# Kernel optimization log

Hardware: AMD Instinct MI355X
Metric: run time of the kernel (lower is better)

## Reference

```python
import jax, jax.numpy as jnp
import numpy as np

HEADS = 8
DIM_HEAD = 40


def setup_inputs() -> dict:
    key = jax.random.key(0)
    ks = jax.random.split(key, 10)
    b, n, j, qd, cd = 8, 4096, 77, 320, 768
    inner = HEADS * DIM_HEAD  # 320
    x = jax.random.normal(ks[0], (b, n, qd), jnp.float32)
    embs = jax.random.normal(ks[1], (b, j, cd), jnp.float32)
    Wq = jax.random.normal(ks[2], (qd, inner), jnp.float32) * 0.02
    Wk = jax.random.normal(ks[3], (cd, inner), jnp.float32) * 0.02
    Wv = jax.random.normal(ks[4], (cd, inner), jnp.float32) * 0.02
    Wo = jax.random.normal(ks[5], (inner, qd), jnp.float32) * 0.02
    bo = jnp.zeros((qd,), jnp.float32)
    # per-query-token, per-key-token additive attention mask (float weights)
    cross_attn_mask = (jax.random.uniform(ks[6], (b, n, j)) < 0.5).astype(jnp.float32)
    strength = jnp.ones((1,), jnp.float32) * 0.8
    # captiontypes >= 0 marks valid key tokens; include some -1 (invalid)
    captiontypes = jax.random.randint(ks[7], (b, j), -1, 3).at[:, 0].set(0)
    global_prompt_mask = (jax.random.uniform(ks[8], (b, j)) > 0.05).at[:, 0].set(True)
    return {"x": x, "embs": embs, "Wq": Wq, "Wk": Wk, "Wv": Wv, "Wo": Wo,
            "bo": bo, "cross_attn_mask": cross_attn_mask, "strength": strength,
            "captiontypes": captiontypes, "global_prompt_mask": global_prompt_mask}


def _split_heads(t):
    # [b, n, h*d] -> [(b h), n, d], head index fastest (matches einops '(b h)')
    b, n, _ = t.shape
    return t.reshape(b, n, HEADS, DIM_HEAD).transpose(0, 2, 1, 3).reshape(b * HEADS, n, DIM_HEAD)


def reference(x, embs, Wq, Wk, Wv, Wo, bo, cross_attn_mask, strength,
              captiontypes, global_prompt_mask):
    b, n, _ = x.shape
    scale = DIM_HEAD ** -0.5
    q = _split_heads(x @ Wq).astype(jnp.float32)   # [(b h), n, d]
    k = _split_heads(embs @ Wk).astype(jnp.float32)  # [(b h), j, d]
    v = _split_heads(embs @ Wv)                      # [(b h), j, d]
    sim = jnp.einsum('bid,bjd->bij', q, k)           # [(b h), n, j] fp32

    NEG = -jnp.finfo(sim.dtype).max
    key_mask = captiontypes >= 0                     # [b, j]
    key_mask_bh = jnp.repeat(key_mask, HEADS, axis=0)[:, None, :]  # [(b h), 1, j]

    # masked std of sim over valid key positions (unbiased, ddof=1), no grad
    w = jnp.broadcast_to(key_mask_bh, sim.shape).astype(sim.dtype)
    cnt = jnp.sum(w)
    mean = jnp.sum(sim * w) / cnt
    var = jnp.sum(w * (sim - mean) ** 2) / (cnt - 1.0)
    simstd = jnp.sqrt(var)

    wf = cross_attn_mask * simstd * strength[0]      # [b, n, j]
    wf = jnp.where(global_prompt_mask[:, None, :], wf, NEG)
    wf = jnp.repeat(wf, HEADS, axis=0)               # [(b h), n, j]
    wf = jax.lax.stop_gradient(wf)

    sim = jnp.where(key_mask_bh, sim, NEG) + wf
    attn = jax.nn.softmax(sim * scale, axis=-1)
    out = jnp.einsum('bij,bjd->bid', attn, v)        # [(b h), n, d]
    out = out.reshape(b, HEADS, n, DIM_HEAD).transpose(0, 2, 1, 3).reshape(b, n, HEADS * DIM_HEAD)
    return out @ Wo + bo
```

## Files before the change

### kernel.cpp

```cpp
#include <hip/hip_runtime.h>
#include <hip/hip_bf16.h>
#include <math.h>

#define HEADS 8
#define DIMH 40
#define BB 8
#define NN 4096
#define JJ 77
#define CDIM 768
#define INNER 320
#define NEGF (-3.4028234663852886e38f)

using bf16 = __hip_bfloat16;
using f32x4 = __attribute__((ext_vector_type(4))) float;
using bf16x8 = __attribute__((ext_vector_type(8))) short;
using ushort8 = __attribute__((ext_vector_type(8))) unsigned short;
using ushort4v = __attribute__((ext_vector_type(4))) unsigned short;

__device__ __forceinline__ unsigned short f2u(float f){
    bf16 t = __float2bfloat16(f);
    return *reinterpret_cast<unsigned short*>(&t);
}
__device__ __forceinline__ float u2f(unsigned short u){
    unsigned int w = ((unsigned int)u) << 16;
    return __uint_as_float(w);
}

struct Stats { int validcnt; int gflag; float simstd; };

__global__ void prep_kernel(const int* ct, const int* gpm, Stats* st){
    __shared__ int sflag, scnt;
    if(threadIdx.x==0){ sflag=0; scnt=0; }
    __syncthreads();
    int lflag=0, lcnt=0;
    for(int i=threadIdx.x;i<154;i+=blockDim.x){
        int g = gpm[i];
        if(g!=0 && g!=1) lflag=1;
    }
    for(int i=threadIdx.x;i<BB*JJ;i+=blockDim.x){
        if(ct[i]>=0) lcnt++;
    }
    if(lflag) atomicOr(&sflag,1);
    atomicAdd(&scnt,lcnt);
    __syncthreads();
    if(threadIdx.x==0){ st->validcnt=scnt; st->gflag=sflag; }
}

__global__ __launch_bounds__(256) void prep_weights(const float* __restrict__ Wq,
                                                    const float* __restrict__ Wo,
                                                    const float* __restrict__ Wk,
                                                    const float* __restrict__ Wv,
                                                    unsigned short* __restrict__ WqT,
                                                    unsigned short* __restrict__ WoT,
                                                    unsigned short* __restrict__ WkvT){
    __shared__ float tile[32][33];
    int blk = blockIdx.x;
    int tx = threadIdx.x & 31, ty = threadIdx.x >> 5;
    if(blk < 200){
        const float* in = (blk<100)? Wq : Wo;
        unsigned short* out = (blk<100)? WqT : WoT;
        int base = (blk<100)? blk : blk-100;
        int bx = base%10, by = base/10;
        int c0 = bx*32, r0 = by*32;
        #pragma unroll
        for(int i=0;i<32;i+=8) tile[ty+i][tx] = in[(size_t)(r0+ty+i)*320 + c0+tx];
        __syncthreads();
        #pragma unroll
        for(int i=0;i<32;i+=8) out[(size_t)(c0+ty+i)*320 + r0+tx] = f2u(tile[tx][ty+i]);
    } else {
        int local = blk-200;
        int nt = local%20, kt = local/20;
        int n0 = nt*32, k0 = kt*32;
        const float* in = (n0<320)? Wk : Wv;
        int nc0 = (n0<320)? n0 : n0-320;
        #pragma unroll
        for(int i=0;i<32;i+=8) tile[ty+i][tx] = in[(size_t)(k0+ty+i)*320 + nc0+tx];
        __syncthreads();
        #pragma unroll
        for(int i=0;i<32;i+=8) WkvT[(size_t)(n0+ty+i)*768 + k0+tx] = f2u(tile[tx][ty+i]);
    }
}

__global__ __launch_bounds__(256) void proj_kv_mfma(const float* __restrict__ embs,
                                                    const unsigned short* __restrict__ WkvT,
                                                    unsigned short* __restrict__ kws,
                                                    unsigned short* __restrict__ vt){
    __shared__ unsigned short As[64][40];
    __shared__ unsigned short Bs[64][40];
    int t = threadIdx.x;
    int bm = blockIdx.x % 10;
    int bn = blockIdx.x / 10;
    int row0 = bm*64, col0 = bn*64;
    int wave=t>>6, lane=t&63, l15=lane&15, lk=lane>>4;

    f32x4 acc[4];
    #pragma unroll
    for(int nf=0;nf<4;nf++) acc[nf]=(f32x4){0.f,0.f,0.f,0.f};

    for(int k0=0;k0<768;k0+=32){
        #pragma unroll
        for(int p=0;p<2;p++){
            int li = (p*256+t)*4; int r = li>>5, kk = li&31;
            int gr = row0 + r;
            ushort4v u;
            if(gr < 616){
                float4 v = *(const float4*)&embs[(size_t)gr*768 + k0+kk];
                u.x=f2u(v.x); u.y=f2u(v.y); u.z=f2u(v.z); u.w=f2u(v.w);
            } else { u.x=0;u.y=0;u.z=0;u.w=0; }
            *(ushort4v*)&As[r][kk] = u;
        }
        {
            int nn = t>>2, kk = (t&3)*8;
            *(ushort8*)&Bs[nn][kk] = *(const ushort8*)&WkvT[(size_t)(col0+nn)*768 + k0+kk];
        }
        __syncthreads();
        bf16x8 aF = *(const bf16x8*)&As[wave*16+l15][lk*8];
        #pragma unroll
        for(int nf=0;nf<4;nf++){
            bf16x8 bF = *(const bf16x8*)&Bs[nf*16+l15][lk*8];
            acc[nf] = __builtin_amdgcn_mfma_f32_16x16x32_bf16(aF,bF,acc[nf],0,0,0);
        }
        __syncthreads();
    }
    #pragma unroll
    for(int nf=0;nf<4;nf++){
        int col = col0 + nf*16 + l15;
        #pragma unroll
        for(int r=0;r<4;r++){
            int m = row0 + wave*16 + lk*4 + r;
            if(m < 616){
                int b = m/77, j = m - 77*b;
                unsigned short val = f2u(acc[nf][r]);
                if(col < 320){
                    int h = col/40, d = col - 40*h;
                    kws[(((size_t)b*HEADS+h)*JJ + j)*DIMH + d] = val;
                } else {
                    int c2 = col-320; int h = c2/40, d = c2 - 40*h;
                    size_t vbase = (((size_t)b*HEADS+h)*DIMH + d)*80;
                    vt[vbase + j] = val;
                    if(j==76){ vt[vbase+77]=0; vt[vbase+78]=0; vt[vbase+79]=0; }
                }
            }
        }
    }
}

template<int A_BF16, int C_F32>
__global__ __launch_bounds__(256) void gemm_mfma(const void* __restrict__ A,
                                                 const unsigned short* __restrict__ Bt,
                                                 const float* __restrict__ bias,
                                                 void* __restrict__ C){
    __shared__ unsigned short As[128][40];
    __shared__ unsigned short Bs[64][40];
    int t = threadIdx.x;
    int bm = blockIdx.x & 255;
    int bn = blockIdx.x >> 8;
    int row0 = bm*128, col0 = bn*64;
    int wave = t>>6, lane = t&63;
    int wm = wave>>1, wn = wave&1;
    int l15 = lane&15, lk = lane>>4;

    f32x4 acc[4][2];
    #pragma unroll
    for(int i=0;i<4;i++)
        #pragma unroll
        for(int j=0;j<2;j++) acc[i][j] = (f32x4){0.f,0.f,0.f,0.f};

    for(int k0=0;k0<320;k0+=32){
        if(A_BF16){
            const unsigned short* Ab = (const unsigned short*)A;
            #pragma unroll
            for(int p=0;p<2;p++){
                int li = (p*256+t)*8; int r = li>>5, kk = li&31;
                *(ushort8*)&As[r][kk] = *(const ushort8*)&Ab[(size_t)(row0+r)*320 + k0+kk];
            }
        } else {
            const float* Af = (const float*)A;
            #pragma unroll
            for(int p=0;p<4;p++){
                int li = (p*256+t)*4; int r = li>>5, kk = li&31;
                float4 v = *(const float4*)&Af[(size_t)(row0+r)*320 + k0+kk];
                ushort4v u; u.x=f2u(v.x); u.y=f2u(v.y); u.z=f2u(v.z); u.w=f2u(v.w);
                *(ushort4v*)&As[r][kk] = u;
            }
        }
        {
            int nn = t>>2, kk = (t&3)*8;
            *(ushort8*)&Bs[nn][kk] = *(const ushort8*)&Bt[(size_t)(col0+nn)*320 + k0+kk];
        }
        __syncthreads();
        bf16x8 a[4], b[2];
        #pragma unroll
        for(int mf=0;mf<4;mf++) a[mf] = *(const bf16x8*)&As[wm*64+mf*16+l15][lk*8];
        #pragma unroll
        for(int nf=0;nf<2;nf++) b[nf] = *(const bf16x8*)&Bs[wn*32+nf*16+l15][lk*8];
        #pragma unroll
        for(int mf=0;mf<4;mf++)
            #pragma unroll
            for(int nf=0;nf<2;nf++)
                acc[mf][nf] = __builtin_amdgcn_mfma_f32_16x16x32_bf16(a[mf], b[nf], acc[mf][nf], 0,0,0);
        __syncthreads();
    }
    if(C_F32){
        float* Cf = (float*)C;
        float bv[2];
        #pragma unroll
        for(int nf=0;nf<2;nf++) bv[nf] = bias[col0+wn*32+nf*16+l15];
        #pragma unroll
        for(int mf=0;mf<4;mf++)
            #pragma unroll
            for(int nf=0;nf<2;nf++){
                int col = col0+wn*32+nf*16+l15;
                #pragma unroll
                for(int r=0;r<4;r++){
                    int m = row0+wm*64+mf*16+lk*4+r;
                    Cf[(size_t)m*320+col] = acc[mf][nf][r] + bv[nf];
                }
            }
    } else {
        unsigned short* Cb = (unsigned short*)C;
        #pragma unroll
        for(int mf=0;mf<4;mf++)
            #pragma unroll
            for(int nf=0;nf<2;nf++){
                int col = col0+wn*32+nf*16+l15;
                #pragma unroll
                for(int r=0;r<4;r++){
                    int m = row0+wm*64+mf*16+lk*4+r;
                    Cb[(size_t)m*320+col] = f2u(acc[mf][nf][r]);
                }
            }
    }
}

__global__ __launch_bounds__(256) void stats_mfma(const unsigned short* __restrict__ qws,
                                                  const unsigned short* __restrict__ kws,
                                                  const int* __restrict__ ct,
                                                  float2* __restrict__ partials){
    int bh = blockIdx.x;
    int b = bh>>3, h = bh&7;
    int t = threadIdx.x;
    int wave=t>>6, lane=t&63, l15=lane&15, lk=lane>>4;
    int wq0 = wave*16;
    bf16x8 zb = {0,0,0,0,0,0,0,0};

    int n0 = blockIdx.y*64;
    size_t qrow = (size_t)(b*NN + n0 + wq0 + l15)*INNER + h*DIMH;
    bf16x8 aF0 = *(const bf16x8*)&qws[qrow + lk*8];
    bf16x8 aF1 = (lk==0) ? *(const bf16x8*)&qws[qrow + 32] : zb;

    bool kv[5];
    bf16x8 bK[2][5];
    #pragma unroll
    for(int jt=0;jt<5;jt++){
        int j = jt*16+l15;
        kv[jt] = (j<JJ) && (ct[b*JJ+j]>=0);
        #pragma unroll
        for(int ks=0;ks<2;ks++){
            if(j<JJ && !(ks==1 && lk>=1))
                bK[ks][jt] = *(const bf16x8*)&kws[((size_t)bh*JJ + j)*DIMH + ks*32 + lk*8];
            else bK[ks][jt] = zb;
        }
    }
    f32x4 sacc[5];
    #pragma unroll
    for(int jt=0;jt<5;jt++) sacc[jt]=(f32x4){0.f,0.f,0.f,0.f};
    #pragma unroll
    for(int jt=0;jt<5;jt++){
        sacc[jt] = __builtin_amdgcn_mfma_f32_16x16x32_bf16(aF0,bK[0][jt],sacc[jt],0,0,0);
        sacc[jt] = __builtin_amdgcn_mfma_f32_16x16x32_bf16(aF1,bK[1][jt],sacc[jt],0,0,0);
    }
    float s1=0.f, s2=0.f;
    #pragma unroll
    for(int jt=0;jt<5;jt++){
        if(kv[jt]){
            #pragma unroll
            for(int r=0;r<4;r++){ float v=sacc[jt][r]; s1+=v; s2+=v*v; }
        }
    }
    #pragma unroll
    for(int off=32;off>0;off>>=1){ s1 += __shfl_down(s1,off); s2 += __shfl_down(s2,off); }
    __shared__ float sa[4], sb[4];
    if(lane==0){ sa[wave]=s1; sb[wave]=s2; }
    __syncthreads();
    if(t==0){
        partials[blockIdx.y*64 + blockIdx.x] =
            make_float2(sa[0]+sa[1]+sa[2]+sa[3], sb[0]+sb[1]+sb[2]+sb[3]);
    }
}

__global__ __launch_bounds__(256) void finalize_kernel(const float2* __restrict__ partials,
                                                       Stats* st){
    int t = threadIdx.x;
    double s1=0.0, s2=0.0;
    for(int i=t;i<4096;i+=256){
        float2 p = partials[i];
        s1 += (double)p.x; s2 += (double)p.y;
    }
    #pragma unroll
    for(int off=32;off>0;off>>=1){ s1 += __shfl_down(s1,off); s2 += __shfl_down(s2,off); }
    __shared__ double da[4], db[4];
    int lane=t&63, w=t>>6;
    if(lane==0){ da[w]=s1; db[w]=s2; }
    __syncthreads();
    if(t==0){
        double S1 = da[0]+da[1]+da[2]+da[3];
        double S2 = db[0]+db[1]+db[2]+db[3];
        double cnt = (double)st->validcnt * HEADS * NN;
        double var = (S2 - S1*S1/cnt)/(cnt-1.0);
        st->simstd = (float)sqrt(var);
    }
}

__global__ __launch_bounds__(256) void attn_mfma(unsigned short* qws,
                                                 const unsigned short* __restrict__ kws,
                                                 const unsigned short* __restrict__ vt,
                                                 const float* __restrict__ cam,
                                                 const float* __restrict__ strength,
                                                 const int* __restrict__ ct,
                                                 const int* __restrict__ gpm,
                                                 const Stats* st){
    int bh = blockIdx.x;
    int b = bh>>3, h = bh&7;
    __shared__ unsigned short P[64][104];
    int t = threadIdx.x;
    int wave=t>>6, lane=t&63, l15=lane&15, lk=lane>>4;
    int wq0 = wave*16;
    bf16x8 zb = {0,0,0,0,0,0,0,0};
    ushort8 z8 = {0,0,0,0,0,0,0,0};

    int n0 = blockIdx.y*64;
    size_t qrow = (size_t)(b*NN + n0 + wq0 + l15)*INNER + h*DIMH;
    bf16x8 aF0 = *(const bf16x8*)&qws[qrow + lk*8];
    bf16x8 aF1 = (lk==0) ? *(const bf16x8*)&qws[qrow + 32] : zb;

    float km[5], gm[5], ad[5];
    float c = st->simstd * strength[0];
    int gflag = st->gflag;
    #pragma unroll
    for(int jt=0;jt<5;jt++){
        int j = jt*16+l15;
        int kvv=0, gv=0;
        if(j<JJ){
            kvv = ct[b*JJ+j]>=0;
            gv = gflag ? (((const unsigned char*)gpm)[b*JJ+j]!=0) : (gpm[b*JJ+j]!=0);
        }
        km[jt] = (j<JJ && kvv)?1.f:0.f;
        ad[jt] = ((j<JJ && kvv)?0.f:NEGF) + ((j<JJ && gv)?0.f:NEGF);
        gm[jt] = (j<JJ && gv)? c : 0.f;
    }
    bf16x8 bK[2][5];
    #pragma unroll
    for(int ks=0;ks<2;ks++)
        #pragma unroll
        for(int jt=0;jt<5;jt++){
            int j = jt*16+l15;
            if(j<JJ && !(ks==1 && lk>=1))
                bK[ks][jt] = *(const bf16x8*)&kws[((size_t)bh*JJ + j)*DIMH + ks*32 + lk*8];
            else bK[ks][jt] = zb;
        }
    bf16x8 bV[3][3];
    #pragma unroll
    for(int ks=0;ks<3;ks++)
        #pragma unroll
        for(int nt=0;nt<3;nt++){
            int d = nt*16+l15;
            if(d<DIMH && !(ks==2 && lk>=2))
                bV[ks][nt] = *(const bf16x8*)&vt[((size_t)bh*DIMH + d)*80 + ks*32 + lk*8];
            else bV[ks][nt] = zb;
        }
    if(t<64){ *(ushort8*)&P[t][80]=z8; *(ushort8*)&P[t][88]=z8; *(ushort8*)&P[t][96]=z8; }

    const float scale = 0.15811388300841897f;
    f32x4 sacc[5];
    #pragma unroll
    for(int jt=0;jt<5;jt++) sacc[jt]=(f32x4){0.f,0.f,0.f,0.f};
    #pragma unroll
    for(int jt=0;jt<5;jt++){
        sacc[jt] = __builtin_amdgcn_mfma_f32_16x16x32_bf16(aF0,bK[0][jt],sacc[jt],0,0,0);
        sacc[jt] = __builtin_amdgcn_mfma_f32_16x16x32_bf16(aF1,bK[1][jt],sacc[jt],0,0,0);
    }
    float lo[5][4];
    #pragma unroll
    for(int jt=0;jt<5;jt++){
        int j = jt*16+l15;
        #pragma unroll
        for(int r=0;r<4;r++){
            int row = n0 + wq0 + 4*lk + r;
            float cv = (j<JJ) ? cam[((size_t)b*NN+row)*JJ + j] : 0.f;
            lo[jt][r] = (sacc[jt][r]*km[jt] + cv*gm[jt] + ad[jt])*scale;
        }
    }
    float dinv[4];
    #pragma unroll
    for(int r=0;r<4;r++){
        float m = lo[0][r];
        #pragma unroll
        for(int jt=1;jt<5;jt++) m = fmaxf(m, lo[jt][r]);
        #pragma unroll
        for(int msk=1;msk<16;msk<<=1) m = fmaxf(m, __shfl_xor(m,msk));
        float s=0.f;
        #pragma unroll
        for(int jt=0;jt<5;jt++){ float e=__expf(lo[jt][r]-m); lo[jt][r]=e; s+=e; }
        #pragma unroll
        for(int msk=1;msk<16;msk<<=1) s += __shfl_xor(s,msk);
        dinv[r]=1.f/s;
    }
    #pragma unroll
    for(int jt=0;jt<5;jt++){
        int j = jt*16+l15;
        #pragma unroll
        for(int r=0;r<4;r++) P[wq0+4*lk+r][j] = f2u(lo[jt][r]*dinv[r]);
    }
    __syncthreads();
    f32x4 oacc[3];
    #pragma unroll
    for(int nt=0;nt<3;nt++) oacc[nt]=(f32x4){0.f,0.f,0.f,0.f};
    #pragma unroll
    for(int ks=0;ks<3;ks++){
        bf16x8 aP = *(const bf16x8*)&P[wq0+l15][ks*32+lk*8];
        #pragma unroll
        for(int nt=0;nt<3;nt++)
            oacc[nt] = __builtin_amdgcn_mfma_f32_16x16x32_bf16(aP,bV[ks][nt],oacc[nt],0,0,0);
    }
    #pragma unroll
    for(int nt=0;nt<3;nt++){
        int d = nt*16+l15;
        #pragma unroll
        for(int r=0;r<4;r++){
            unsigned short ush = f2u(oacc[nt][r]);
            int other = __shfl_xor((int)ush, 1);
            if((l15&1)==0 && d<DIMH){
                unsigned int word = (unsigned int)ush | (((unsigned int)(unsigned short)other)<<16);
                int row = n0 + wq0 + 4*lk + r;
                *(unsigned int*)&qws[(size_t)(b*NN+row)*INNER + h*DIMH + d] = word;
            }
        }
    }
}

extern "C" void kernel_launch(void* const* d_in, const int* in_sizes, int n_in,
                              void* d_out, int out_size, void* d_ws, size_t ws_size,
                              hipStream_t stream) {
    const float* x        = (const float*)d_in[0];
    const float* embs     = (const float*)d_in[1];
    const float* Wq       = (const float*)d_in[2];
    const float* Wk       = (const float*)d_in[3];
    const float* Wv       = (const float*)d_in[4];
    const float* Wo       = (const float*)d_in[5];
    const float* bo       = (const float*)d_in[6];
    const float* cam      = (const float*)d_in[7];
    const float* strength = (const float*)d_in[8];
    const int*  ct       = (const int*)d_in[9];
    const int*  gpm      = (const int*)d_in[10];

    char* ws = (char*)d_ws;
    unsigned short* qws  = (unsigned short*)ws;
    unsigned short* kws  = (unsigned short*)(ws + 20971520);
    unsigned short* vt   = (unsigned short*)(ws + 21365760);
    unsigned short* WqT  = (unsigned short*)(ws + 21775360);
    unsigned short* WoT  = (unsigned short*)(ws + 21980160);
    unsigned short* WkvT = (unsigned short*)(ws + 22184960);
    Stats* st  = (Stats*)(ws + 23168000);
    float2* partials = (float2*)(ws + 23169024);

    prep_kernel<<<1,256,0,stream>>>(ct,gpm,st);
    prep_weights<<<680,256,0,stream>>>(Wq,Wo,Wk,Wv,WqT,WoT,WkvT);
    proj_kv_mfma<<<100,256,0,stream>>>(embs,WkvT,kws,vt);
    gemm_mfma<0,0><<<1280,256,0,stream>>>(x,WqT,nullptr,qws);
    stats_mfma<<<dim3(64,64),256,0,stream>>>(qws,kws,ct,partials);
    finalize_kernel<<<1,256,0,stream>>>(partials,st);
    attn_mfma<<<dim3(64,64),256,0,stream>>>(qws,kws,vt,cam,strength,ct,gpm,st);
    gemm_mfma<1,1><<<1280,256,0,stream>>>(qws,WoT,bo,d_out);
}
```

Baseline: 134.0 us.

## Store Q/attention output head-major and precompute per-key mask tables

The Q projection now writes Q in a [(b h), n, d] head-major layout, so stats and attention kernels read each head's 64-row tile contiguously instead of striding by 320 elements. The output GEMM gathers its A operand from that layout. The finalize kernel now builds per-batch key-mask, additive-offset and global-mask tables once, and attention loads them instead of recomputing from captiontypes and the prompt mask in every block. Attention also issues its cross-attention-mask loads before the QK MFMAs to overlap their latency. The risk is that the scattered 2-byte stores in the Q GEMM epilogue and the gathered loads in the output GEMM may cost more than the attention-side gains.

```diff
diff --git a/kernel.cpp b/kernel.cpp
--- a/kernel.cpp
+++ b/kernel.cpp
@@ -145,7 +145,7 @@
     }
 }
 
-template<int A_BF16, int C_F32>
+template<int A_MODE, int C_MODE>
 __global__ __launch_bounds__(256) void gemm_mfma(const void* __restrict__ A,
                                                  const unsigned short* __restrict__ Bt,
                                                  const float* __restrict__ bias,
@@ -167,12 +167,15 @@
         for(int j=0;j<2;j++) acc[i][j] = (f32x4){0.f,0.f,0.f,0.f};
 
     for(int k0=0;k0<320;k0+=32){
-        if(A_BF16){
+        if(A_MODE==2){
             const unsigned short* Ab = (const unsigned short*)A;
             #pragma unroll
             for(int p=0;p<2;p++){
                 int li = (p*256+t)*8; int r = li>>5, kk = li&31;
-                *(ushort8*)&As[r][kk] = *(const ushort8*)&Ab[(size_t)(row0+r)*320 + k0+kk];
+                int m = row0+r; int k = k0+kk;
+                int b = m>>12, n = m&4095;
+                int h = k/40, d = k-40*h;
+                *(ushort8*)&As[r][kk] = *(const ushort8*)&Ab[(((size_t)(b*8+h))*NN + n)*DIMH + d];
             }
         } else {
             const float* Af = (const float*)A;
@@ -201,7 +204,7 @@
                 acc[mf][nf] = __builtin_amdgcn_mfma_f32_16x16x32_bf16(a[mf], b[nf], acc[mf][nf], 0,0,0);
         __syncthreads();
     }
-    if(C_F32){
+    if(C_MODE==1){
         float* Cf = (float*)C;
         float bv[2];
         #pragma unroll
@@ -224,30 +227,32 @@
             #pragma unroll
             for(int nf=0;nf<2;nf++){
                 int col = col0+wn*32+nf*16+l15;
+                int h = col/40, d = col-40*h;
                 #pragma unroll
                 for(int r=0;r<4;r++){
                     int m = row0+wm*64+mf*16+lk*4+r;
-                    Cb[(size_t)m*320+col] = f2u(acc[mf][nf][r]);
+                    int b = m>>12, n = m&4095;
+                    Cb[(((size_t)(b*8+h))*NN + n)*DIMH + d] = f2u(acc[mf][nf][r]);
                 }
             }
     }
 }
 
-__global__ __launch_bounds__(256) void stats_mfma(const unsigned short* __restrict__ qws,
+__global__ __launch_bounds__(256) void stats_mfma(const unsigned short* __restrict__ qh,
                                                   const unsigned short* __restrict__ kws,
                                                   const int* __restrict__ ct,
                                                   float2* __restrict__ partials){
     int bh = blockIdx.x;
-    int b = bh>>3, h = bh&7;
+    int b = bh>>3;
     int t = threadIdx.x;
     int wave=t>>6, lane=t&63, l15=lane&15, lk=lane>>4;
     int wq0 = wave*16;
     bf16x8 zb = {0,0,0,0,0,0,0,0};
 
     int n0 = blockIdx.y*64;
-    size_t qrow = (size_t)(b*NN + n0 + wq0 + l15)*INNER + h*DIMH;
-    bf16x8 aF0 = *(const bf16x8*)&qws[qrow + lk*8];
-    bf16x8 aF1 = (lk==0) ? *(const bf16x8*)&qws[qrow + 32] : zb;
+    size_t qrow = ((size_t)bh*NN + n0 + wq0 + l15)*DIMH;
+    bf16x8 aF0 = *(const bf16x8*)&qh[qrow + lk*8];
+    bf16x8 aF1 = (lk==0) ? *(const bf16x8*)&qh[qrow + 32] : zb;
 
     bool kv[5];
     bf16x8 bK[2][5];
@@ -290,7 +295,13 @@
 }
 
 __global__ __launch_bounds__(256) void finalize_kernel(const float2* __restrict__ partials,
-                                                       Stats* st){
+                                                       const int* __restrict__ ct,
+                                                       const int* __restrict__ gpm,
+                                                       const float* __restrict__ strength,
+                                                       Stats* st,
+                                                       float* __restrict__ kmT,
+                                                       float* __restrict__ adT,
+                                                       float* __restrict__ gmT){
     int t = threadIdx.x;
     double s1=0.0, s2=0.0;
     for(int i=t;i<4096;i+=256){
@@ -300,6 +311,7 @@
     #pragma unroll
     for(int off=32;off>0;off>>=1){ s1 += __shfl_down(s1,off); s2 += __shfl_down(s2,off); }
     __shared__ double da[4], db[4];
+    __shared__ float s_simstd;
     int lane=t&63, w=t>>6;
     if(lane==0){ da[w]=s1; db[w]=s2; }
     __syncthreads();
@@ -308,20 +320,35 @@
         double S2 = db[0]+db[1]+db[2]+db[3];
         double cnt = (double)st->validcnt * HEADS * NN;
         double var = (S2 - S1*S1/cnt)/(cnt-1.0);
-        st->simstd = (float)sqrt(var);
-    }
-}
-
-__global__ __launch_bounds__(256) void attn_mfma(unsigned short* qws,
+        float sd = (float)sqrt(var);
+        st->simstd = sd;
+        s_simstd = sd;
+    }
+    __syncthreads();
+    float c = s_simstd * strength[0];
+    int gflag = st->gflag;
+    for(int i=t;i<BB*80;i+=256){
+        int b = i/80, j = i-80*b;
+        int kvv=0, gv=0;
+        if(j<JJ){
+            kvv = ct[b*JJ+j]>=0;
+            gv = gflag ? (((const unsigned char*)gpm)[b*JJ+j]!=0) : (gpm[b*JJ+j]!=0);
+        }
+        kmT[i] = (j<JJ && kvv)?1.f:0.f;
+        adT[i] = ((j<JJ && kvv)?0.f:NEGF) + ((j<JJ && gv)?0.f:NEGF);
+        gmT[i] = (j<JJ && gv)? c : 0.f;
+    }
+}
+
+__global__ __launch_bounds__(256) void attn_mfma(unsigned short* qh,
                                                  const unsigned short* __restrict__ kws,
                                                  const unsigned short* __restrict__ vt,
                                                  const float* __restrict__ cam,
-                                                 const float* __restrict__ strength,
-                                                 const int* __restrict__ ct,
-                                                 const int* __restrict__ gpm,
-                                                 const Stats* st){
+                                                 const float* __restrict__ kmT,
+                                                 const float* __restrict__ adT,
+                                                 const float* __restrict__ gmT){
     int bh = blockIdx.x;
-    int b = bh>>3, h = bh&7;
+    int b = bh>>3;
     __shared__ unsigned short P[64][104];
     int t = threadIdx.x;
     int wave=t>>6, lane=t&63, l15=lane&15, lk=lane>>4;
@@ -330,24 +357,25 @@
     ushort8 z8 = {0,0,0,0,0,0,0,0};
 
     int n0 = blockIdx.y*64;
-    size_t qrow = (size_t)(b*NN + n0 + wq0 + l15)*INNER + h*DIMH;
-    bf16x8 aF0 = *(const bf16x8*)&qws[qrow + lk*8];
-    bf16x8 aF1 = (lk==0) ? *(const bf16x8*)&qws[qrow + 32] : zb;
-
+    size_t qrow = ((size_t)bh*NN + n0 + wq0 + l15)*DIMH;
+    bf16x8 aF0 = *(const bf16x8*)&qh[qrow + lk*8];
+    bf16x8 aF1 = (lk==0) ? *(const bf16x8*)&qh[qrow + 32] : zb;
+
+    float cv[5][4];
+    #pragma unroll
+    for(int jt=0;jt<5;jt++){
+        int j = jt*16+l15; int jc = (j<JJ)? j : 76;
+        #pragma unroll
+        for(int r=0;r<4;r++){
+            int row = n0 + wq0 + 4*lk + r;
+            cv[jt][r] = cam[((size_t)b*NN+row)*JJ + jc];
+        }
+    }
     float km[5], gm[5], ad[5];
-    float c = st->simstd * strength[0];
-    int gflag = st->gflag;
     #pragma unroll
     for(int jt=0;jt<5;jt++){
         int j = jt*16+l15;
-        int kvv=0, gv=0;
-        if(j<JJ){
-            kvv = ct[b*JJ+j]>=0;
-            gv = gflag ? (((const unsigned char*)gpm)[b*JJ+j]!=0) : (gpm[b*JJ+j]!=0);
-        }
-        km[jt] = (j<JJ && kvv)?1.f:0.f;
-        ad[jt] = ((j<JJ && kvv)?0.f:NEGF) + ((j<JJ && gv)?0.f:NEGF);
-        gm[jt] = (j<JJ && gv)? c : 0.f;
+        km[jt] = kmT[b*80+j]; ad[jt] = adT[b*80+j]; gm[jt] = gmT[b*80+j];
     }
     bf16x8 bK[2][5];
     #pragma unroll
@@ -383,13 +411,9 @@
     float lo[5][4];
     #pragma unroll
     for(int jt=0;jt<5;jt++){
-        int j = jt*16+l15;
-        #pragma unroll
-        for(int r=0;r<4;r++){
-            int row = n0 + wq0 + 4*lk + r;
-            float cv = (j<JJ) ? cam[((size_t)b*NN+row)*JJ + j] : 0.f;
-            lo[jt][r] = (sacc[jt][r]*km[jt] + cv*gm[jt] + ad[jt])*scale;
-        }
+        #pragma unroll
+        for(int r=0;r<4;r++)
+            lo[jt][r] = (sacc[jt][r]*km[jt] + cv[jt][r]*gm[jt] + ad[jt])*scale;
     }
     float dinv[4];
     #pragma unroll
@@ -433,7 +457,7 @@
             if((l15&1)==0 && d<DIMH){
                 unsigned int word = (unsigned int)ush | (((unsigned int)(unsigned short)other)<<16);
                 int row = n0 + wq0 + 4*lk + r;
-                *(unsigned int*)&qws[(size_t)(b*NN+row)*INNER + h*DIMH + d] = word;
+                *(unsigned int*)&qh[((size_t)bh*NN + row)*DIMH + d] = word;
             }
         }
     }
@@ -455,7 +479,7 @@
     const int*  gpm      = (const int*)d_in[10];
 
     char* ws = (char*)d_ws;
-    unsigned short* qws  = (unsigned short*)ws;
+    unsigned short* qh   = (unsigned short*)ws;
     unsigned short* kws  = (unsigned short*)(ws + 20971520);
     unsigned short* vt   = (unsigned short*)(ws + 21365760);
     unsigned short* WqT  = (unsigned short*)(ws + 21775360);
@@ -463,13 +487,16 @@
     unsigned short* WkvT = (unsigned short*)(ws + 22184960);
     Stats* st  = (Stats*)(ws + 23168000);
     float2* partials = (float2*)(ws + 23169024);
+    float* kmT = (float*)(ws + 23201792);
+    float* adT = (float*)(ws + 23204352);
+    float* gmT = (float*)(ws + 23206912);
 
     prep_kernel<<<1,256,0,stream>>>(ct,gpm,st);
     prep_weights<<<680,256,0,stream>>>(Wq,Wo,Wk,Wv,WqT,WoT,WkvT);
     proj_kv_mfma<<<100,256,0,stream>>>(embs,WkvT,kws,vt);
-    gemm_mfma<0,0><<<1280,256,0,stream>>>(x,WqT,nullptr,qws);
-    stats_mfma<<<dim3(64,64),256,0,stream>>>(qws,kws,ct,partials);
-    finalize_kernel<<<1,256,0,stream>>>(partials,st);
-    attn_mfma<<<dim3(64,64),256,0,stream>>>(qws,kws,vt,cam,strength,ct,gpm,st);
-    gemm_mfma<1,1><<<1280,256,0,stream>>>(qws,WoT,bo,d_out);
-}
+    gemm_mfma<0,2><<<1280,256,0,stream>>>(x,WqT,nullptr,qh);
+    stats_mfma<<<dim3(64,64),256,0,stream>>>(qh,kws,ct,partials);
+    finalize_kernel<<<1,256,0,stream>>>(partials,ct,gpm,strength,st,kmT,adT,gmT);
+    attn_mfma<<<dim3(64,64),256,0,stream>>>(qh,kws,vt,cam,kmT,adT,gmT);
+    gemm_mfma<2,1><<<1280,256,0,stream>>>(qh,WoT,bo,d_out);
+}
```

Measured after the change: 130.2 us. 2.9% less time.
